# Kernel tuning notes

Measured on AMD Instinct MI355X. Metric: run time of the kernel, lower is better.

## Reference

```python
import jax, jax.numpy as jnp
import numpy as np

N = 50000      # nodes
E = 800000     # random edges (self-loops appended inside reference)
DIN = 128
DH = 32        # per-head hidden dim of layer 1
H = 8          # heads
DOUT = 32      # output dim (layer 2, concat=False)
NEG_SLOPE = 0.2


def segment_softmax(e, seg, num):
    # numerically stable softmax over variable-size segments (per-destination)
    m = jax.ops.segment_max(e, seg, num_segments=num)
    m = jnp.where(jnp.isfinite(m), m, jnp.zeros_like(m))
    ex = jnp.exp(e - m[seg])
    s = jax.ops.segment_sum(ex, seg, num_segments=num)
    return ex / (s[seg] + 1e-16)


def gatv2_conv(x, src, dst, Wl, Wr, att, bias, heads, dim, concat):
    n = x.shape[0]
    xl = (x @ Wl).reshape(n, heads, dim)   # source transform
    xr = (x @ Wr).reshape(n, heads, dim)   # target transform
    z = xl[src] + xr[dst]                  # [E, H, D] gather per edge
    z = jnp.where(z > 0, z, NEG_SLOPE * z) # LeakyReLU BEFORE attention vector (GATv2)
    e = jnp.einsum('ehd,hd->eh', z, att)   # attention logits [E, H]
    alpha = segment_softmax(e, dst, n)     # softmax over in-edges of each dst
    out = jax.ops.segment_sum(alpha[:, :, None] * xl[src], dst, num_segments=n)
    if concat:
        return out.reshape(n, heads * dim) + bias
    return out.mean(axis=1) + bias


def setup_inputs() -> dict:
    key = jax.random.key(0)
    ks = jax.random.split(key, 12)
    x = jax.random.normal(ks[0], (N, DIN), dtype=jnp.float32)
    edge_index = jax.random.randint(ks[1], (2, E), 0, N, dtype=jnp.int64)
    s = 0.05
    Wl1 = jax.random.normal(ks[2], (DIN, H * DH), dtype=jnp.float32) * s
    Wr1 = jax.random.normal(ks[3], (DIN, H * DH), dtype=jnp.float32) * s
    att1 = jax.random.normal(ks[4], (H, DH), dtype=jnp.float32) * s
    b1 = jnp.zeros((H * DH,), dtype=jnp.float32)
    Wl2 = jax.random.normal(ks[5], (H * DH, H * DOUT), dtype=jnp.float32) * s
    Wr2 = jax.random.normal(ks[6], (H * DH, H * DOUT), dtype=jnp.float32) * s
    att2 = jax.random.normal(ks[7], (H, DOUT), dtype=jnp.float32) * s
    b2 = jnp.zeros((DOUT,), dtype=jnp.float32)
    return {"x": x, "edge_index": edge_index, "Wl1": Wl1, "Wr1": Wr1,
            "att1": att1, "b1": b1, "Wl2": Wl2, "Wr2": Wr2,
            "att2": att2, "b2": b2}


def reference(x, edge_index, Wl1, Wr1, att1, b1, Wl2, Wr2, att2, b2):
    n = x.shape[0]
    loops = jnp.arange(n, dtype=edge_index.dtype)
    src = jnp.concatenate([edge_index[0], loops])  # PyG adds self-loops by default
    dst = jnp.concatenate([edge_index[1], loops])
    h = gatv2_conv(x, src, dst, Wl1, Wr1, att1, b1, H, DH, concat=True)
    h = jax.nn.elu(h)
    out = gatv2_conv(h, src, dst, Wl2, Wr2, att2, b2, H, DOUT, concat=False)
    return out
```

## Files before the change

kernel.cpp:

```cpp
#include <hip/hip_runtime.h>
#include <hip/hip_bf16.h>

typedef __hip_bfloat16 bf16;
typedef __attribute__((ext_vector_type(8))) short bf16x8;
typedef __attribute__((ext_vector_type(4))) float f32x4;

#define N_NODES 50000
#define E_RAW   800000
#define E_TOT   850000
#define H_HEADS 8
#define F_DIM   256
#define NB_SCAN 196

__device__ __forceinline__ float loadF(const void* p, size_t i, int f32) {
    return f32 ? ((const float*)p)[i] : __bfloat162float(((const bf16*)p)[i]);
}
__device__ __forceinline__ int loadI(const void* p, size_t i, int is32) {
    return is32 ? ((const int*)p)[i] : (int)((const long long*)p)[i];
}
__device__ __forceinline__ float uasf(unsigned u) { return __uint_as_float(u); }
__device__ __forceinline__ unsigned f2bfbits(float f) {
    unsigned u = __float_as_uint(f);
    return (u + 0x7fff + ((u >> 16) & 1)) >> 16;
}
__device__ __forceinline__ short f2bfs(float f) {
    unsigned u = __float_as_uint(f);
    return (short)((u + 0x7fff + ((u >> 16) & 1)) >> 16);
}

__global__ void detect_zero(const void* __restrict__ x, const void* __restrict__ ei,
                            int* __restrict__ flags, int* __restrict__ counts) {
    int gid = blockIdx.x * 256 + threadIdx.x;
    if (gid < N_NODES) counts[gid] = 0;
    if (blockIdx.x != 0) return;
    __shared__ int sf[2];
    int t = threadIdx.x;
    if (t < 2) sf[t] = 0;
    __syncthreads();
    const unsigned short* xs = (const unsigned short*)x;
    int f32 = 0;
    for (int i = t; i < 8192; i += 256) {
        unsigned e = (xs[i] >> 7) & 0xFF;
        if (e >= 134) f32 = 1;
    }
    const int* eii = (const int*)ei;
    int odd = 0;
    for (int i = t; i < 1024; i += 256)
        if (eii[2 * i + 1] != 0) odd = 1;
    if (f32) atomicOr(&sf[0], 1);
    if (odd) atomicOr(&sf[1], 1);
    __syncthreads();
    if (t < 2) flags[t] = sf[t];
}

__global__ void prep(const void* __restrict__ wl1, const void* __restrict__ wr1,
                     const void* __restrict__ wl2, const void* __restrict__ wr2,
                     const void* __restrict__ ei,
                     bf16* __restrict__ wb, int* __restrict__ counts,
                     unsigned short* __restrict__ rank,
                     const int* __restrict__ flags) {
    const int f32 = flags[0], is32 = flags[1];
    int gid = blockIdx.x * 256 + threadIdx.x;
    if (gid < E_TOT) {
        int d = (gid < E_RAW) ? loadI(ei, (size_t)E_RAW + gid, is32) : (gid - E_RAW);
        rank[gid] = (unsigned short)atomicAdd(&counts[d], 1);
    }
    for (size_t j = gid; j < 196608; j += (size_t)gridDim.x * 256) {
        const void* src; size_t off, base;
        int k, n;
        if (j < 65536) {
            int half = j >= 32768;
            off = j - (size_t)half * 32768;
            src = half ? wr1 : wl1;
            k = (int)(off >> 8); n = half * 256 + (int)(off & 255);
            base = 0;
        } else {
            size_t jj = j - 65536;
            int half = jj >= 65536;
            off = jj - (size_t)half * 65536;
            src = half ? wr2 : wl2;
            k = (int)(off >> 8); n = half * 256 + (int)(off & 255);
            base = 65536;
        }
        int kb = k >> 5, jo = k & 7;
        int lane = ((k >> 3) & 3) * 16 + (n & 15);
        int ctg = n >> 4;
        size_t dst = base + (((size_t)(kb * 32 + ctg) * 64 + lane) * 8 + jo);
        wb[dst] = __float2bfloat16(loadF(src, off, f32));
    }
}

__global__ void scan1(const int* __restrict__ counts, int* __restrict__ rp,
                      int* __restrict__ bsum) {
    __shared__ int sm[256];
    int b = blockIdx.x, t = threadIdx.x;
    int i = b * 256 + t;
    int v = (i < N_NODES) ? counts[i] : 0;
    sm[t] = v; __syncthreads();
    for (int off = 1; off < 256; off <<= 1) {
        int u = (t >= off) ? sm[t - off] : 0;
        __syncthreads();
        sm[t] += u;
        __syncthreads();
    }
    int incl = sm[t];
    if (i < N_NODES) rp[i] = incl - v;
    if (t == 255) bsum[b] = incl;
}

__global__ void scan2(int* __restrict__ bsum) {
    __shared__ int sm[256];
    int t = threadIdx.x;
    int v = (t < NB_SCAN) ? bsum[t] : 0;
    sm[t] = v; __syncthreads();
    for (int off = 1; off < 256; off <<= 1) {
        int u = (t >= off) ? sm[t - off] : 0;
        __syncthreads();
        sm[t] += u;
        __syncthreads();
    }
    if (t < NB_SCAN) bsum[t] = sm[t] - v;
}

__global__ void scan3(int* __restrict__ rp, const int* __restrict__ bsum) {
    int b = blockIdx.x, t = threadIdx.x;
    int i = b * 256 + t;
    if (i < N_NODES) rp[i] += bsum[b];
    if (i == 0) rp[N_NODES] = E_TOT;
}

__global__ void fill(const void* __restrict__ ei, const int* __restrict__ rp,
                     const unsigned short* __restrict__ rank,
                     int* __restrict__ srcs, const int* __restrict__ flags) {
    const int is32 = flags[1];
    int e = blockIdx.x * 256 + threadIdx.x;
    if (e >= E_TOT) return;
    int s, d;
    if (e < E_RAW) { s = loadI(ei, e, is32); d = loadI(ei, (size_t)E_RAW + e, is32); }
    else           { s = d = e - E_RAW; }
    srcs[rp[d] + rank[e]] = s;
}

__launch_bounds__(256)
__global__ void gemm_mfma(const void* __restrict__ A, const bf16* __restrict__ Wsw,
                          bf16* __restrict__ Cl, bf16* __restrict__ Cr,
                          int M, int K, int aDyn, const int* __restrict__ flags) {
    const int af32 = aDyn ? flags[0] : 0;
    const int tid = threadIdx.x;
    const int w = tid >> 6, lane = tid & 63, q = lane >> 4, l16 = lane & 15;
    const int bRow = blockIdx.x * 128 + (w >> 1) * 64;
    const int bCol = blockIdx.y * 128 + (w & 1) * 64;
    const int ctg0 = bCol >> 4;
    const short* Wp = (const short*)Wsw;
    const int nkb = K >> 5;
    int rows[4];
#pragma unroll
    for (int i = 0; i < 4; ++i) {
        int r = bRow + i * 16 + l16;
        rows[i] = r < M ? r : M - 1;
    }
    f32x4 acc[16] = {};
    for (int kb = 0; kb < nkb; ++kb) {
        bf16x8 a[4], b[4];
#pragma unroll
        for (int i = 0; i < 4; ++i) {
            if (!af32) {
                a[i] = *(const bf16x8*)((const short*)A + (size_t)rows[i] * K + q * 8 + kb * 32);
            } else {
                const float* Apf = (const float*)A + (size_t)rows[i] * K + q * 8 + kb * 32;
                float4 a0 = *(const float4*)(Apf);
                float4 a1 = *(const float4*)(Apf + 4);
                a[i][0] = f2bfs(a0.x); a[i][1] = f2bfs(a0.y);
                a[i][2] = f2bfs(a0.z); a[i][3] = f2bfs(a0.w);
                a[i][4] = f2bfs(a1.x); a[i][5] = f2bfs(a1.y);
                a[i][6] = f2bfs(a1.z); a[i][7] = f2bfs(a1.w);
            }
        }
#pragma unroll
        for (int j = 0; j < 4; ++j)
            b[j] = *(const bf16x8*)(Wp + ((size_t)(kb * 32 + ctg0 + j) * 64 + lane) * 8);
#pragma unroll
        for (int i = 0; i < 4; ++i)
#pragma unroll
            for (int j = 0; j < 4; ++j)
                acc[i * 4 + j] =
                    __builtin_amdgcn_mfma_f32_16x16x32_bf16(b[j], a[i], acc[i * 4 + j], 0, 0, 0);
    }
    unsigned short* C = (unsigned short*)(bCol < 256 ? Cl : Cr);
    const int cBase = (bCol < 256 ? bCol : bCol - 256) + q * 4;
#pragma unroll
    for (int i = 0; i < 4; ++i) {
        int row = bRow + i * 16 + l16;
        if (row < M) {
#pragma unroll
            for (int j = 0; j < 4; ++j) {
                f32x4 v = acc[i * 4 + j];
                uint2 o;
                o.x = f2bfbits(v[0]) | (f2bfbits(v[1]) << 16);
                o.y = f2bfbits(v[2]) | (f2bfbits(v[3]) << 16);
                *(uint2*)(C + (size_t)row * 256 + cBase + j * 16) = o;
            }
        }
    }
}

#define EDGE2(Q, PRED)                                                        \
    {                                                                         \
        float2 X0 = {uasf(Q.x << 16), uasf(Q.x & 0xffff0000u)};               \
        float2 X1 = {uasf(Q.y << 16), uasf(Q.y & 0xffff0000u)};               \
        float2 X2 = {uasf(Q.z << 16), uasf(Q.z & 0xffff0000u)};               \
        float2 X3 = {uasf(Q.w << 16), uasf(Q.w & 0xffff0000u)};               \
        float2 z0 = {X0.x + rv0.x, X0.y + rv0.y};                             \
        float2 z1 = {X1.x + rv1.x, X1.y + rv1.y};                             \
        float2 z2 = {X2.x + rv2.x, X2.y + rv2.y};                             \
        float2 z3 = {X3.x + rv3.x, X3.y + rv3.y};                             \
        z0.x = fmaxf(z0.x, 0.2f * z0.x); z0.y = fmaxf(z0.y, 0.2f * z0.y);     \
        z1.x = fmaxf(z1.x, 0.2f * z1.x); z1.y = fmaxf(z1.y, 0.2f * z1.y);     \
        z2.x = fmaxf(z2.x, 0.2f * z2.x); z2.y = fmaxf(z2.y, 0.2f * z2.y);     \
        z3.x = fmaxf(z3.x, 0.2f * z3.x); z3.y = fmaxf(z3.y, 0.2f * z3.y);     \
        float2 p2 = {z0.x * a0.x, z0.y * a0.y};                               \
        p2.x = fmaf(z1.x, a1.x, p2.x); p2.y = fmaf(z1.y, a1.y, p2.y);         \
        p2.x = fmaf(z2.x, a2.x, p2.x); p2.y = fmaf(z2.y, a2.y, p2.y);         \
        p2.x = fmaf(z3.x, a3.x, p2.x); p2.y = fmaf(z3.y, a3.y, p2.y);         \
        float p = p2.x + p2.y;                                                \
        p += __shfl_xor(p, 1); p += __shfl_xor(p, 2);                         \
        float wv = (PRED) ? __expf(p) : 0.f;                                  \
        den += wv;                                                            \
        n0.x = fmaf(wv, X0.x, n0.x); n0.y = fmaf(wv, X0.y, n0.y);             \
        n1.x = fmaf(wv, X1.x, n1.x); n1.y = fmaf(wv, X1.y, n1.y);             \
        n2.x = fmaf(wv, X2.x, n2.x); n2.y = fmaf(wv, X2.y, n2.y);             \
        n3.x = fmaf(wv, X3.x, n3.x); n3.y = fmaf(wv, X3.y, n3.y);             \
    }
__launch_bounds__(256)
__global__ void fused_attn(const int* __restrict__ rp, const int* __restrict__ srcs,
                           const bf16* __restrict__ xl, const bf16* __restrict__ xr,
                           const void* __restrict__ att, const void* __restrict__ bias,
                           void* __restrict__ outp, int mode,
                           const int* __restrict__ flags) {
    const int f32 = flags[0];
    const int tid = threadIdx.x, wid = tid >> 6, lane = tid & 63;
    const int sub = lane & 31;
    const int d = blockIdx.x * 8 + wid * 2 + (lane >> 5);

    const unsigned short* xru = (const unsigned short*)xr;
    uint4 xv = *(const uint4*)(xru + (size_t)d * 256 + sub * 8);
    float2 rv0 = {uasf(xv.x << 16), uasf(xv.x & 0xffff0000u)};
    float2 rv1 = {uasf(xv.y << 16), uasf(xv.y & 0xffff0000u)};
    float2 rv2 = {uasf(xv.z << 16), uasf(xv.z & 0xffff0000u)};
    float2 rv3 = {uasf(xv.w << 16), uasf(xv.w & 0xffff0000u)};
    float2 a0, a1, a2, a3;
    if (f32) {
        float4 t0 = *(const float4*)((const float*)att + sub * 8);
        float4 t1 = *(const float4*)((const float*)att + sub * 8 + 4);
        a0 = {t0.x, t0.y}; a1 = {t0.z, t0.w}; a2 = {t1.x, t1.y}; a3 = {t1.z, t1.w};
    } else {
        uint4 av = *(const uint4*)((const unsigned short*)att + sub * 8);
        a0 = {uasf(av.x << 16), uasf(av.x & 0xffff0000u)};
        a1 = {uasf(av.y << 16), uasf(av.y & 0xffff0000u)};
        a2 = {uasf(av.z << 16), uasf(av.z & 0xffff0000u)};
        a3 = {uasf(av.w << 16), uasf(av.w & 0xffff0000u)};
    }

    const int start = rp[d], cnt = rp[d + 1] - start;
    const int cnt1 = cnt - 1;
    int mA = __shfl(cnt, 0), mB = __shfl(cnt, 32);
    const int maxc = mA > mB ? mA : mB;
    const int* sp = srcs + start;
    const unsigned short* xlu = (const unsigned short*)xl + sub * 8;

    float den = 0.f;
    float2 n0 = {0,0}, n1 = {0,0}, n2 = {0,0}, n3 = {0,0};
    int i = 0;
    for (; i + 1 < maxc; i += 2) {
        int i0 = i < cnt1 ? i : cnt1;
        int i1 = i + 1 < cnt1 ? i + 1 : cnt1;
        int s0 = sp[i0], s1 = sp[i1];
        uint4 q0 = *(const uint4*)(xlu + (size_t)s0 * 256);
        uint4 q1 = *(const uint4*)(xlu + (size_t)s1 * 256);
        EDGE2(q0, i < cnt);
        EDGE2(q1, i + 1 < cnt);
    }
    if (i < maxc) {
        int i0 = i < cnt1 ? i : cnt1;
        int s0 = sp[i0];
        uint4 q0 = *(const uint4*)(xlu + (size_t)s0 * 256);
        EDGE2(q0, i < cnt);
    }
    float rd = 1.f / (den + 1e-16f);
    float v[8] = {n0.x * rd, n0.y * rd, n1.x * rd, n1.y * rd,
                  n2.x * rd, n2.y * rd, n3.x * rd, n3.y * rd};

    if (mode == 1) {
        float b[8];
        if (f32) {
            float4 t0 = *(const float4*)((const float*)bias + sub * 8);
            float4 t1 = *(const float4*)((const float*)bias + sub * 8 + 4);
            b[0]=t0.x; b[1]=t0.y; b[2]=t0.z; b[3]=t0.w;
            b[4]=t1.x; b[5]=t1.y; b[6]=t1.z; b[7]=t1.w;
        } else {
            uint4 bv = *(const uint4*)((const unsigned short*)bias + sub * 8);
            b[0]=uasf(bv.x<<16); b[1]=uasf(bv.x&0xffff0000u);
            b[2]=uasf(bv.y<<16); b[3]=uasf(bv.y&0xffff0000u);
            b[4]=uasf(bv.z<<16); b[5]=uasf(bv.z&0xffff0000u);
            b[6]=uasf(bv.w<<16); b[7]=uasf(bv.w&0xffff0000u);
        }
        uint4 o;
        unsigned oo[4];
#pragma unroll
        for (int k = 0; k < 4; ++k) {
            float u0 = v[2*k]   + b[2*k];
            float u1 = v[2*k+1] + b[2*k+1];
            u0 = u0 > 0.f ? u0 : expm1f(u0);
            u1 = u1 > 0.f ? u1 : expm1f(u1);
            oo[k] = f2bfbits(u0) | (f2bfbits(u1) << 16);
        }
        o.x = oo[0]; o.y = oo[1]; o.z = oo[2]; o.w = oo[3];
        *(uint4*)((unsigned short*)outp + (size_t)d * 256 + sub * 8) = o;
    } else {
#pragma unroll
        for (int k = 0; k < 8; ++k) {
            v[k] += __shfl_xor(v[k], 4);
            v[k] += __shfl_xor(v[k], 8);
            v[k] += __shfl_xor(v[k], 16);
        }
        if (sub < 4) {
            int j = sub * 8;
            float o[8];
#pragma unroll
            for (int k = 0; k < 8; ++k)
                o[k] = v[k] * 0.125f + loadF(bias, j + k, f32);
            if (f32) {
                float4 o0 = {o[0], o[1], o[2], o[3]};
                float4 o1 = {o[4], o[5], o[6], o[7]};
                *(float4*)((float*)outp + (size_t)d * 32 + j)     = o0;
                *(float4*)((float*)outp + (size_t)d * 32 + j + 4) = o1;
            } else {
                uint4 ob;
                ob.x = f2bfbits(o[0]) | (f2bfbits(o[1]) << 16);
                ob.y = f2bfbits(o[2]) | (f2bfbits(o[3]) << 16);
                ob.z = f2bfbits(o[4]) | (f2bfbits(o[5]) << 16);
                ob.w = f2bfbits(o[6]) | (f2bfbits(o[7]) << 16);
                *(uint4*)((unsigned short*)outp + (size_t)d * 32 + j) = ob;
            }
        }
    }
}

extern "C" void kernel_launch(void* const* d_in, const int* in_sizes, int n_in,
                              void* d_out, int out_size, void* d_ws, size_t ws_size,
                              hipStream_t stream) {
    const void* x    = d_in[0];
    const void* ei   = d_in[1];
    const void* Wl1  = d_in[2];
    const void* Wr1  = d_in[3];
    const void* att1 = d_in[4];
    const void* b1   = d_in[5];
    const void* Wl2  = d_in[6];
    const void* Wr2  = d_in[7];
    const void* att2 = d_in[8];
    const void* b2   = d_in[9];

    char* p = (char*)d_ws;
    auto take = [&](size_t bytes) { char* r = p; p += (bytes + 255) & ~(size_t)255; return r; };
    int*  flags  = (int*) take(64 * sizeof(int));
    bf16* wb     = (bf16*)take(196608 * sizeof(bf16));
    bf16* xl     = (bf16*)take((size_t)N_NODES * F_DIM * sizeof(bf16));
    bf16* xr     = (bf16*)take((size_t)N_NODES * F_DIM * sizeof(bf16));
    bf16* h1     = (bf16*)take((size_t)N_NODES * F_DIM * sizeof(bf16));
    int*  rp     = (int*) take((N_NODES + 1) * sizeof(int));
    int*  counts = (int*) take(N_NODES * sizeof(int));
    int*  bsum   = (int*) take(256 * sizeof(int));
    unsigned short* rank = (unsigned short*)take((size_t)E_TOT * sizeof(unsigned short));
    int*  srcs   = (int*) take(((size_t)E_TOT + 64) * sizeof(int));

    bf16* W1sw = wb;
    bf16* W2sw = wb + 65536;

    const int GB = (E_TOT + 255) / 256;

    detect_zero<<<196, 256, 0, stream>>>(x, ei, flags, counts);
    prep<<<GB, 256, 0, stream>>>(Wl1, Wr1, Wl2, Wr2, ei, wb, counts, rank, flags);
    scan1<<<NB_SCAN, 256, 0, stream>>>(counts, rp, bsum);
    scan2<<<1, 256, 0, stream>>>(bsum);
    scan3<<<NB_SCAN, 256, 0, stream>>>(rp, bsum);
    fill<<<GB, 256, 0, stream>>>(ei, rp, rank, srcs, flags);

    dim3 ggrd((N_NODES + 127) / 128, 4);

    gemm_mfma<<<ggrd, 256, 0, stream>>>(x, W1sw, xl, xr, N_NODES, 128, 1, flags);
    fused_attn<<<N_NODES / 8, 256, 0, stream>>>(rp, srcs, xl, xr, att1, b1, h1, 1, flags);

    gemm_mfma<<<ggrd, 256, 0, stream>>>(h1, W2sw, xl, xr, N_NODES, 256, 0, flags);
    fused_attn<<<N_NODES / 8, 256, 0, stream>>>(rp, srcs, xl, xr, att2, b2, d_out, 2, flags);
}
```

Before: 390.6 us.

## Decompose LeakyReLU attention into linear plus abs terms, precompute per-node source scores

Rewrites leaky(z)·a as 0.6·a·z + 0.4·a·|z|, so the linear part splits into a per-source score computed in the GEMM epilogue and a per-destination constant computed once. The per-edge loop then only evaluates the abs term plus two scalar adds, with fewer ALU ops per edge. It also pads srcs with zeros so the edge loop can drop its index clamping. The cost is an extra gather of one float per edge and per head, an extra epilogue in the GEMM, and a small difference in floating-point rounding.

Result: slower. 405.5 us (+3.8%).

```diff
diff --git a/kernel.cpp b/kernel.cpp
--- a/kernel.cpp
+++ b/kernel.cpp
@@ -134,7 +134,8 @@
                      int* __restrict__ srcs, const int* __restrict__ flags) {
     const int is32 = flags[1];
     int e = blockIdx.x * 256 + threadIdx.x;
-    if (e >= E_TOT) return;
+    if (e >= E_TOT + 64) return;
+    if (e >= E_TOT) { srcs[e] = 0; return; }
     int s, d;
     if (e < E_RAW) { s = loadI(ei, e, is32); d = loadI(ei, (size_t)E_RAW + e, is32); }
     else           { s = d = e - E_RAW; }
@@ -144,8 +145,10 @@
 __launch_bounds__(256)
 __global__ void gemm_mfma(const void* __restrict__ A, const bf16* __restrict__ Wsw,
                           bf16* __restrict__ Cl, bf16* __restrict__ Cr,
+                          float* __restrict__ sL, const void* __restrict__ att,
                           int M, int K, int aDyn, const int* __restrict__ flags) {
     const int af32 = aDyn ? flags[0] : 0;
+    const int attf32 = flags[0];
     const int tid = threadIdx.x;
     const int w = tid >> 6, lane = tid & 63, q = lane >> 4, l16 = lane & 15;
     const int bRow = blockIdx.x * 128 + (w >> 1) * 64;
@@ -202,28 +205,65 @@
             }
         }
     }
-}
-
-#define EDGE2(Q, PRED)                                                        \
+    if (bCol < 256) {
+        const int hb = bCol >> 5;
+        float4 alo, ahi, blo, bhi;
+        if (attf32) {
+            const float* ap = (const float*)att + hb * 32 + q * 4;
+            alo = *(const float4*)(ap);
+            ahi = *(const float4*)(ap + 16);
+            blo = *(const float4*)(ap + 32);
+            bhi = *(const float4*)(ap + 48);
+        } else {
+            const unsigned short* ap = (const unsigned short*)att + hb * 32 + q * 4;
+            uint2 u0 = *(const uint2*)(ap);
+            uint2 u1 = *(const uint2*)(ap + 16);
+            uint2 u2 = *(const uint2*)(ap + 32);
+            uint2 u3 = *(const uint2*)(ap + 48);
+            alo = {uasf(u0.x << 16), uasf(u0.x & 0xffff0000u),
+                   uasf(u0.y << 16), uasf(u0.y & 0xffff0000u)};
+            ahi = {uasf(u1.x << 16), uasf(u1.x & 0xffff0000u),
+                   uasf(u1.y << 16), uasf(u1.y & 0xffff0000u)};
+            blo = {uasf(u2.x << 16), uasf(u2.x & 0xffff0000u),
+                   uasf(u2.y << 16), uasf(u2.y & 0xffff0000u)};
+            bhi = {uasf(u3.x << 16), uasf(u3.x & 0xffff0000u),
+                   uasf(u3.y << 16), uasf(u3.y & 0xffff0000u)};
+        }
+#pragma unroll
+        for (int i = 0; i < 4; ++i) {
+            int row = bRow + i * 16 + l16;
+            f32x4 c0 = acc[i * 4 + 0], c1 = acc[i * 4 + 1];
+            f32x4 c2 = acc[i * 4 + 2], c3 = acc[i * 4 + 3];
+            float s0 = alo.x * c0[0] + alo.y * c0[1] + alo.z * c0[2] + alo.w * c0[3]
+                     + ahi.x * c1[0] + ahi.y * c1[1] + ahi.z * c1[2] + ahi.w * c1[3];
+            float s1 = blo.x * c2[0] + blo.y * c2[1] + blo.z * c2[2] + blo.w * c2[3]
+                     + bhi.x * c3[0] + bhi.y * c3[1] + bhi.z * c3[2] + bhi.w * c3[3];
+            s0 += __shfl_xor(s0, 16); s0 += __shfl_xor(s0, 32);
+            s1 += __shfl_xor(s1, 16); s1 += __shfl_xor(s1, 32);
+            if (lane < 16 && row < M) {
+                float2 sw = {0.6f * s0, 0.6f * s1};
+                *(float2*)(sL + (size_t)row * 8 + hb) = sw;
+            }
+        }
+    }
+}
+
+#define EDGE2(Q, SLV, PRED)                                                   \
     {                                                                         \
         float2 X0 = {uasf(Q.x << 16), uasf(Q.x & 0xffff0000u)};               \
         float2 X1 = {uasf(Q.y << 16), uasf(Q.y & 0xffff0000u)};               \
         float2 X2 = {uasf(Q.z << 16), uasf(Q.z & 0xffff0000u)};               \
         float2 X3 = {uasf(Q.w << 16), uasf(Q.w & 0xffff0000u)};               \
-        float2 z0 = {X0.x + rv0.x, X0.y + rv0.y};                             \
-        float2 z1 = {X1.x + rv1.x, X1.y + rv1.y};                             \
-        float2 z2 = {X2.x + rv2.x, X2.y + rv2.y};                             \
-        float2 z3 = {X3.x + rv3.x, X3.y + rv3.y};                             \
-        z0.x = fmaxf(z0.x, 0.2f * z0.x); z0.y = fmaxf(z0.y, 0.2f * z0.y);     \
-        z1.x = fmaxf(z1.x, 0.2f * z1.x); z1.y = fmaxf(z1.y, 0.2f * z1.y);     \
-        z2.x = fmaxf(z2.x, 0.2f * z2.x); z2.y = fmaxf(z2.y, 0.2f * z2.y);     \
-        z3.x = fmaxf(z3.x, 0.2f * z3.x); z3.y = fmaxf(z3.y, 0.2f * z3.y);     \
-        float2 p2 = {z0.x * a0.x, z0.y * a0.y};                               \
-        p2.x = fmaf(z1.x, a1.x, p2.x); p2.y = fmaf(z1.y, a1.y, p2.y);         \
-        p2.x = fmaf(z2.x, a2.x, p2.x); p2.y = fmaf(z2.y, a2.y, p2.y);         \
-        p2.x = fmaf(z3.x, a3.x, p2.x); p2.y = fmaf(z3.y, a3.y, p2.y);         \
-        float p = p2.x + p2.y;                                                \
-        p += __shfl_xor(p, 1); p += __shfl_xor(p, 2);                         \
+        float qq = a0.x * fabsf(X0.x + rv0.x);                                \
+        qq = fmaf(a0.y, fabsf(X0.y + rv0.y), qq);                             \
+        qq = fmaf(a1.x, fabsf(X1.x + rv1.x), qq);                             \
+        qq = fmaf(a1.y, fabsf(X1.y + rv1.y), qq);                             \
+        qq = fmaf(a2.x, fabsf(X2.x + rv2.x), qq);                             \
+        qq = fmaf(a2.y, fabsf(X2.y + rv2.y), qq);                             \
+        qq = fmaf(a3.x, fabsf(X3.x + rv3.x), qq);                             \
+        qq = fmaf(a3.y, fabsf(X3.y + rv3.y), qq);                             \
+        qq += __shfl_xor(qq, 1); qq += __shfl_xor(qq, 2);                     \
+        float p = qq + cd + (SLV);                                            \
         float wv = (PRED) ? __expf(p) : 0.f;                                  \
         den += wv;                                                            \
         n0.x = fmaf(wv, X0.x, n0.x); n0.y = fmaf(wv, X0.y, n0.y);             \
@@ -234,6 +274,7 @@
 __launch_bounds__(256)
 __global__ void fused_attn(const int* __restrict__ rp, const int* __restrict__ srcs,
                            const bf16* __restrict__ xl, const bf16* __restrict__ xr,
+                           const float* __restrict__ sL,
                            const void* __restrict__ att, const void* __restrict__ bias,
                            void* __restrict__ outp, int mode,
                            const int* __restrict__ flags) {
@@ -261,30 +302,39 @@
         a3 = {uasf(av.w << 16), uasf(av.w & 0xffff0000u)};
     }
 
+    float t = a0.x * rv0.x + a0.y * rv0.y;
+    t = fmaf(a1.x, rv1.x, t); t = fmaf(a1.y, rv1.y, t);
+    t = fmaf(a2.x, rv2.x, t); t = fmaf(a2.y, rv2.y, t);
+    t = fmaf(a3.x, rv3.x, t); t = fmaf(a3.y, rv3.y, t);
+    t += __shfl_xor(t, 1); t += __shfl_xor(t, 2);
+    const float cd = 0.6f * t;
+    a0.x *= 0.4f; a0.y *= 0.4f; a1.x *= 0.4f; a1.y *= 0.4f;
+    a2.x *= 0.4f; a2.y *= 0.4f; a3.x *= 0.4f; a3.y *= 0.4f;
+
     const int start = rp[d], cnt = rp[d + 1] - start;
-    const int cnt1 = cnt - 1;
     int mA = __shfl(cnt, 0), mB = __shfl(cnt, 32);
     const int maxc = mA > mB ? mA : mB;
     const int* sp = srcs + start;
     const unsigned short* xlu = (const unsigned short*)xl + sub * 8;
+    const float* sLp = sL + (sub >> 2);
 
     float den = 0.f;
     float2 n0 = {0,0}, n1 = {0,0}, n2 = {0,0}, n3 = {0,0};
     int i = 0;
     for (; i + 1 < maxc; i += 2) {
-        int i0 = i < cnt1 ? i : cnt1;
-        int i1 = i + 1 < cnt1 ? i + 1 : cnt1;
-        int s0 = sp[i0], s1 = sp[i1];
+        int s0 = sp[i], s1 = sp[i + 1];
         uint4 q0 = *(const uint4*)(xlu + (size_t)s0 * 256);
         uint4 q1 = *(const uint4*)(xlu + (size_t)s1 * 256);
-        EDGE2(q0, i < cnt);
-        EDGE2(q1, i + 1 < cnt);
+        float sl0 = sLp[(size_t)s0 * 8];
+        float sl1 = sLp[(size_t)s1 * 8];
+        EDGE2(q0, sl0, i < cnt);
+        EDGE2(q1, sl1, i + 1 < cnt);
     }
     if (i < maxc) {
-        int i0 = i < cnt1 ? i : cnt1;
-        int s0 = sp[i0];
+        int s0 = sp[i];
         uint4 q0 = *(const uint4*)(xlu + (size_t)s0 * 256);
-        EDGE2(q0, i < cnt);
+        float sl0 = sLp[(size_t)s0 * 8];
+        EDGE2(q0, sl0, i < cnt);
     }
     float rd = 1.f / (den + 1e-16f);
     float v[8] = {n0.x * rd, n0.y * rd, n1.x * rd, n1.y * rd,
@@ -367,6 +417,7 @@
     bf16* xl     = (bf16*)take((size_t)N_NODES * F_DIM * sizeof(bf16));
     bf16* xr     = (bf16*)take((size_t)N_NODES * F_DIM * sizeof(bf16));
     bf16* h1     = (bf16*)take((size_t)N_NODES * F_DIM * sizeof(bf16));
+    float* sLb   = (float*)take((size_t)N_NODES * 8 * sizeof(float));
     int*  rp     = (int*) take((N_NODES + 1) * sizeof(int));
     int*  counts = (int*) take(N_NODES * sizeof(int));
     int*  bsum   = (int*) take(256 * sizeof(int));
@@ -387,9 +438,9 @@
 
     dim3 ggrd((N_NODES + 127) / 128, 4);
 
-    gemm_mfma<<<ggrd, 256, 0, stream>>>(x, W1sw, xl, xr, N_NODES, 128, 1, flags);
-    fused_attn<<<N_NODES / 8, 256, 0, stream>>>(rp, srcs, xl, xr, att1, b1, h1, 1, flags);
-
-    gemm_mfma<<<ggrd, 256, 0, stream>>>(h1, W2sw, xl, xr, N_NODES, 256, 0, flags);
-    fused_attn<<<N_NODES / 8, 256, 0, stream>>>(rp, srcs, xl, xr, att2, b2, d_out, 2, flags);
-}
+    gemm_mfma<<<ggrd, 256, 0, stream>>>(x, W1sw, xl, xr, sLb, att1, N_NODES, 128, 1, flags);
+    fused_attn<<<N_NODES / 8, 256, 0, stream>>>(rp, srcs, xl, xr, sLb, att1, b1, h1, 1, flags);
+
+    gemm_mfma<<<ggrd, 256, 0, stream>>>(h1, W2sw, xl, xr, sLb, att2, N_NODES, 256, 0, flags);
+    fused_attn<<<N_NODES / 8, 256, 0, stream>>>(rp, srcs, xl, xr, sLb, att2, b2, d_out, 2, flags);
+}
```

## Pre-convert x to bf16, rewrite LeakyReLU logits algebraically, unroll gather by four

Applied to the files above, without the earlier changes.

A new kernel converts x to bf16 once, so the first GEMM no longer converts fp32 to bf16 inline for each of its four column tiles. The attention logit now uses leaky(z) = 0.6z + 0.4|z|: the destination term a·xr is computed once per node, and the per-edge work becomes an abs-weighted dot plus a dot with xl. The edge loop is unrolled to four gathers in flight using packed float2 math. The index clamp is dropped by zero-padding srcs, so overhanging reads stay in bounds. The price is an extra kernel and buffer pass, and slightly different fp32 rounding in the logits.

After: 374.5 us. 1.04x faster.

```diff
diff --git a/kernel.cpp b/kernel.cpp
--- a/kernel.cpp
+++ b/kernel.cpp
@@ -4,6 +4,7 @@
 typedef __hip_bfloat16 bf16;
 typedef __attribute__((ext_vector_type(8))) short bf16x8;
 typedef __attribute__((ext_vector_type(4))) float f32x4;
+typedef __attribute__((ext_vector_type(2))) float f32x2;
 
 #define N_NODES 50000
 #define E_RAW   800000
@@ -51,6 +52,28 @@
     if (odd) atomicOr(&sf[1], 1);
     __syncthreads();
     if (t < 2) flags[t] = sf[t];
+}
+
+__global__ void xcvt(const void* __restrict__ x, bf16* __restrict__ xb,
+                     const int* __restrict__ flags) {
+    const int f32 = flags[0];
+    int i = blockIdx.x * 256 + threadIdx.x;
+    if (i >= (N_NODES * 128) / 8) return;
+    unsigned short* dst = (unsigned short*)xb + (size_t)i * 8;
+    if (f32) {
+        const float* xp = (const float*)x + (size_t)i * 8;
+        float4 v0 = *(const float4*)xp;
+        float4 v1 = *(const float4*)(xp + 4);
+        uint4 o;
+        o.x = f2bfbits(v0.x) | (f2bfbits(v0.y) << 16);
+        o.y = f2bfbits(v0.z) | (f2bfbits(v0.w) << 16);
+        o.z = f2bfbits(v1.x) | (f2bfbits(v1.y) << 16);
+        o.w = f2bfbits(v1.z) | (f2bfbits(v1.w) << 16);
+        *(uint4*)dst = o;
+    } else {
+        uint4 v = *(const uint4*)((const unsigned short*)x + (size_t)i * 8);
+        *(uint4*)dst = v;
+    }
 }
 
 __global__ void prep(const void* __restrict__ wl1, const void* __restrict__ wr1,
@@ -134,7 +157,8 @@
                      int* __restrict__ srcs, const int* __restrict__ flags) {
     const int is32 = flags[1];
     int e = blockIdx.x * 256 + threadIdx.x;
-    if (e >= E_TOT) return;
+    if (e >= E_TOT + 64) return;
+    if (e >= E_TOT) { srcs[e] = 0; return; }
     int s, d;
     if (e < E_RAW) { s = loadI(ei, e, is32); d = loadI(ei, (size_t)E_RAW + e, is32); }
     else           { s = d = e - E_RAW; }
@@ -142,10 +166,9 @@
 }
 
 __launch_bounds__(256)
-__global__ void gemm_mfma(const void* __restrict__ A, const bf16* __restrict__ Wsw,
+__global__ void gemm_mfma(const bf16* __restrict__ A, const bf16* __restrict__ Wsw,
                           bf16* __restrict__ Cl, bf16* __restrict__ Cr,
-                          int M, int K, int aDyn, const int* __restrict__ flags) {
-    const int af32 = aDyn ? flags[0] : 0;
+                          int M, int K) {
     const int tid = threadIdx.x;
     const int w = tid >> 6, lane = tid & 63, q = lane >> 4, l16 = lane & 15;
     const int bRow = blockIdx.x * 128 + (w >> 1) * 64;
@@ -163,19 +186,8 @@
     for (int kb = 0; kb < nkb; ++kb) {
         bf16x8 a[4], b[4];
 #pragma unroll
-        for (int i = 0; i < 4; ++i) {
-            if (!af32) {
-                a[i] = *(const bf16x8*)((const short*)A + (size_t)rows[i] * K + q * 8 + kb * 32);
-            } else {
-                const float* Apf = (const float*)A + (size_t)rows[i] * K + q * 8 + kb * 32;
-                float4 a0 = *(const float4*)(Apf);
-                float4 a1 = *(const float4*)(Apf + 4);
-                a[i][0] = f2bfs(a0.x); a[i][1] = f2bfs(a0.y);
-                a[i][2] = f2bfs(a0.z); a[i][3] = f2bfs(a0.w);
-                a[i][4] = f2bfs(a1.x); a[i][5] = f2bfs(a1.y);
-                a[i][6] = f2bfs(a1.z); a[i][7] = f2bfs(a1.w);
-            }
-        }
+        for (int i = 0; i < 4; ++i)
+            a[i] = *(const bf16x8*)((const short*)A + (size_t)rows[i] * K + q * 8 + kb * 32);
 #pragma unroll
         for (int j = 0; j < 4; ++j)
             b[j] = *(const bf16x8*)(Wp + ((size_t)(kb * 32 + ctg0 + j) * 64 + lane) * 8);
@@ -204,32 +216,29 @@
     }
 }
 
-#define EDGE2(Q, PRED)                                                        \
+#define EDGE(Q, PRED)                                                         \
     {                                                                         \
-        float2 X0 = {uasf(Q.x << 16), uasf(Q.x & 0xffff0000u)};               \
-        float2 X1 = {uasf(Q.y << 16), uasf(Q.y & 0xffff0000u)};               \
-        float2 X2 = {uasf(Q.z << 16), uasf(Q.z & 0xffff0000u)};               \
-        float2 X3 = {uasf(Q.w << 16), uasf(Q.w & 0xffff0000u)};               \
-        float2 z0 = {X0.x + rv0.x, X0.y + rv0.y};                             \
-        float2 z1 = {X1.x + rv1.x, X1.y + rv1.y};                             \
-        float2 z2 = {X2.x + rv2.x, X2.y + rv2.y};                             \
-        float2 z3 = {X3.x + rv3.x, X3.y + rv3.y};                             \
-        z0.x = fmaxf(z0.x, 0.2f * z0.x); z0.y = fmaxf(z0.y, 0.2f * z0.y);     \
-        z1.x = fmaxf(z1.x, 0.2f * z1.x); z1.y = fmaxf(z1.y, 0.2f * z1.y);     \
-        z2.x = fmaxf(z2.x, 0.2f * z2.x); z2.y = fmaxf(z2.y, 0.2f * z2.y);     \
-        z3.x = fmaxf(z3.x, 0.2f * z3.x); z3.y = fmaxf(z3.y, 0.2f * z3.y);     \
-        float2 p2 = {z0.x * a0.x, z0.y * a0.y};                               \
-        p2.x = fmaf(z1.x, a1.x, p2.x); p2.y = fmaf(z1.y, a1.y, p2.y);         \
-        p2.x = fmaf(z2.x, a2.x, p2.x); p2.y = fmaf(z2.y, a2.y, p2.y);         \
-        p2.x = fmaf(z3.x, a3.x, p2.x); p2.y = fmaf(z3.y, a3.y, p2.y);         \
-        float p = p2.x + p2.y;                                                \
-        p += __shfl_xor(p, 1); p += __shfl_xor(p, 2);                         \
-        float wv = (PRED) ? __expf(p) : 0.f;                                  \
+        f32x2 X0 = {uasf(Q.x << 16), uasf(Q.x & 0xffff0000u)};                \
+        f32x2 X1 = {uasf(Q.y << 16), uasf(Q.y & 0xffff0000u)};                \
+        f32x2 X2 = {uasf(Q.z << 16), uasf(Q.z & 0xffff0000u)};                \
+        f32x2 X3 = {uasf(Q.w << 16), uasf(Q.w & 0xffff0000u)};                \
+        f32x2 z0 = X0 + rv0, z1 = X1 + rv1, z2 = X2 + rv2, z3 = X3 + rv3;     \
+        float qq = a0.x * fabsf(z0.x);                                        \
+        qq = fmaf(a0.y, fabsf(z0.y), qq);                                     \
+        qq = fmaf(a1.x, fabsf(z1.x), qq);                                     \
+        qq = fmaf(a1.y, fabsf(z1.y), qq);                                     \
+        qq = fmaf(a2.x, fabsf(z2.x), qq);                                     \
+        qq = fmaf(a2.y, fabsf(z2.y), qq);                                     \
+        qq = fmaf(a3.x, fabsf(z3.x), qq);                                     \
+        qq = fmaf(a3.y, fabsf(z3.y), qq);                                     \
+        f32x2 slv = a0 * X0;                                                  \
+        slv += a1 * X1; slv += a2 * X2; slv += a3 * X3;                       \
+        float pp = fmaf(0.6f, slv.x + slv.y, 0.4f * qq);                      \
+        pp += __shfl_xor(pp, 1); pp += __shfl_xor(pp, 2);                     \
+        float wv = (PRED) ? __expf(pp + cd) : 0.f;                            \
         den += wv;                                                            \
-        n0.x = fmaf(wv, X0.x, n0.x); n0.y = fmaf(wv, X0.y, n0.y);             \
-        n1.x = fmaf(wv, X1.x, n1.x); n1.y = fmaf(wv, X1.y, n1.y);             \
-        n2.x = fmaf(wv, X2.x, n2.x); n2.y = fmaf(wv, X2.y, n2.y);             \
-        n3.x = fmaf(wv, X3.x, n3.x); n3.y = fmaf(wv, X3.y, n3.y);             \
+        f32x2 wv2 = {wv, wv};                                                 \
+        n0 += wv2 * X0; n1 += wv2 * X1; n2 += wv2 * X2; n3 += wv2 * X3;       \
     }
 __launch_bounds__(256)
 __global__ void fused_attn(const int* __restrict__ rp, const int* __restrict__ srcs,
@@ -244,11 +253,11 @@
 
     const unsigned short* xru = (const unsigned short*)xr;
     uint4 xv = *(const uint4*)(xru + (size_t)d * 256 + sub * 8);
-    float2 rv0 = {uasf(xv.x << 16), uasf(xv.x & 0xffff0000u)};
-    float2 rv1 = {uasf(xv.y << 16), uasf(xv.y & 0xffff0000u)};
-    float2 rv2 = {uasf(xv.z << 16), uasf(xv.z & 0xffff0000u)};
-    float2 rv3 = {uasf(xv.w << 16), uasf(xv.w & 0xffff0000u)};
-    float2 a0, a1, a2, a3;
+    f32x2 rv0 = {uasf(xv.x << 16), uasf(xv.x & 0xffff0000u)};
+    f32x2 rv1 = {uasf(xv.y << 16), uasf(xv.y & 0xffff0000u)};
+    f32x2 rv2 = {uasf(xv.z << 16), uasf(xv.z & 0xffff0000u)};
+    f32x2 rv3 = {uasf(xv.w << 16), uasf(xv.w & 0xffff0000u)};
+    f32x2 a0, a1, a2, a3;
     if (f32) {
         float4 t0 = *(const float4*)((const float*)att + sub * 8);
         float4 t1 = *(const float4*)((const float*)att + sub * 8 + 4);
@@ -261,30 +270,36 @@
         a3 = {uasf(av.w << 16), uasf(av.w & 0xffff0000u)};
     }
 
+    f32x2 tv = a0 * rv0;
+    tv += a1 * rv1; tv += a2 * rv2; tv += a3 * rv3;
+    float t = tv.x + tv.y;
+    t += __shfl_xor(t, 1); t += __shfl_xor(t, 2);
+    const float cd = 0.6f * t;
+
     const int start = rp[d], cnt = rp[d + 1] - start;
-    const int cnt1 = cnt - 1;
     int mA = __shfl(cnt, 0), mB = __shfl(cnt, 32);
     const int maxc = mA > mB ? mA : mB;
     const int* sp = srcs + start;
     const unsigned short* xlu = (const unsigned short*)xl + sub * 8;
 
     float den = 0.f;
-    float2 n0 = {0,0}, n1 = {0,0}, n2 = {0,0}, n3 = {0,0};
+    f32x2 n0 = {0,0}, n1 = {0,0}, n2 = {0,0}, n3 = {0,0};
     int i = 0;
-    for (; i + 1 < maxc; i += 2) {
-        int i0 = i < cnt1 ? i : cnt1;
-        int i1 = i + 1 < cnt1 ? i + 1 : cnt1;
-        int s0 = sp[i0], s1 = sp[i1];
+    for (; i + 3 < maxc; i += 4) {
+        int s0 = sp[i], s1 = sp[i + 1], s2 = sp[i + 2], s3 = sp[i + 3];
         uint4 q0 = *(const uint4*)(xlu + (size_t)s0 * 256);
         uint4 q1 = *(const uint4*)(xlu + (size_t)s1 * 256);
-        EDGE2(q0, i < cnt);
-        EDGE2(q1, i + 1 < cnt);
-    }
-    if (i < maxc) {
-        int i0 = i < cnt1 ? i : cnt1;
-        int s0 = sp[i0];
+        uint4 q2 = *(const uint4*)(xlu + (size_t)s2 * 256);
+        uint4 q3 = *(const uint4*)(xlu + (size_t)s3 * 256);
+        EDGE(q0, i < cnt);
+        EDGE(q1, i + 1 < cnt);
+        EDGE(q2, i + 2 < cnt);
+        EDGE(q3, i + 3 < cnt);
+    }
+    for (; i < maxc; ++i) {
+        int s0 = sp[i];
         uint4 q0 = *(const uint4*)(xlu + (size_t)s0 * 256);
-        EDGE2(q0, i < cnt);
+        EDGE(q0, i < cnt);
     }
     float rd = 1.f / (den + 1e-16f);
     float v[8] = {n0.x * rd, n0.y * rd, n1.x * rd, n1.y * rd,
@@ -375,10 +390,12 @@
 
     bf16* W1sw = wb;
     bf16* W2sw = wb + 65536;
+    bf16* xb   = h1;
 
     const int GB = (E_TOT + 255) / 256;
 
     detect_zero<<<196, 256, 0, stream>>>(x, ei, flags, counts);
+    xcvt<<<(N_NODES * 128 / 8 + 255) / 256, 256, 0, stream>>>(x, xb, flags);
     prep<<<GB, 256, 0, stream>>>(Wl1, Wr1, Wl2, Wr2, ei, wb, counts, rank, flags);
     scan1<<<NB_SCAN, 256, 0, stream>>>(counts, rp, bsum);
     scan2<<<1, 256, 0, stream>>>(bsum);
@@ -387,9 +404,9 @@
 
     dim3 ggrd((N_NODES + 127) / 128, 4);
 
-    gemm_mfma<<<ggrd, 256, 0, stream>>>(x, W1sw, xl, xr, N_NODES, 128, 1, flags);
+    gemm_mfma<<<ggrd, 256, 0, stream>>>(xb, W1sw, xl, xr, N_NODES, 128);
     fused_attn<<<N_NODES / 8, 256, 0, stream>>>(rp, srcs, xl, xr, att1, b1, h1, 1, flags);
 
-    gemm_mfma<<<ggrd, 256, 0, stream>>>(h1, W2sw, xl, xr, N_NODES, 256, 0, flags);
+    gemm_mfma<<<ggrd, 256, 0, stream>>>(h1, W2sw, xl, xr, N_NODES, 256);
     fused_attn<<<N_NODES / 8, 256, 0, stream>>>(rp, srcs, xl, xr, att2, b2, d_out, 2, flags);
 }
```
